# Optimization experiments

Hardware: AMD Instinct MI355X
Metric: run time of the kernel (lower is better)

The kernel has to match this reference:

```python
import jax, jax.numpy as jnp
import numpy as np

VOCAB, H, E, B, S = 50257, 1024, 1024, 64, 2048


def setup_inputs() -> dict:
    key = jax.random.key(0)
    ks = jax.random.split(key, 12)
    s = 0.02
    return {
        "input_seq": jax.random.randint(ks[0], (B,), 0, VOCAB),
        "last_hidden": jax.random.normal(ks[1], (1, B, H), jnp.float32),
        "last_cell": jax.random.normal(ks[2], (1, B, H), jnp.float32),
        "encoder_outputs": jax.random.normal(ks[3], (S, B, H), jnp.float32),
        "emb_W": jax.random.normal(ks[4], (VOCAB, E), jnp.float32) * s,
        "W_ih": jax.random.normal(ks[5], (4 * H, E), jnp.float32) * s,
        "W_hh": jax.random.normal(ks[6], (4 * H, H), jnp.float32) * s,
        "b_ih": jnp.zeros((4 * H,), jnp.float32),
        "b_hh": jnp.zeros((4 * H,), jnp.float32),
        "concat_W": jax.random.normal(ks[7], (H, 2 * H), jnp.float32) * s,
        "concat_b": jnp.zeros((H,), jnp.float32),
        "out_W": jax.random.normal(ks[8], (VOCAB, H), jnp.float32) * s,
        "out_b": jnp.zeros((VOCAB,), jnp.float32),
    }


def reference(input_seq, last_hidden, last_cell, encoder_outputs,
              emb_W, W_ih, W_hh, b_ih, b_hh,
              concat_W, concat_b, out_W, out_b):
    # Embedding lookup (dropout is identity in eval mode)
    x = emb_W[input_seq]                      # [B, E]
    h0 = last_hidden[0]                       # [B, H]
    c0 = last_cell[0]                         # [B, H]
    # Single LSTM step (PyTorch gate order: i, f, g, o)
    gates = x @ W_ih.T + b_ih + h0 @ W_hh.T + b_hh   # [B, 4H]
    i, f, g, o = jnp.split(gates, 4, axis=-1)
    c = jax.nn.sigmoid(f) * c0 + jax.nn.sigmoid(i) * jnp.tanh(g)
    h = jax.nn.sigmoid(o) * jnp.tanh(c)       # [B, H] == rnn_output
    # 'dot' attention: energies[b, s] = h[b] . enc[s, b]  (vectorized)
    energies = jnp.einsum('bh,sbh->bs', h, encoder_outputs)   # [B, S]
    attn = jax.nn.softmax(energies, axis=1)                   # [B, S]
    context = jnp.einsum('bs,sbh->bh', attn, encoder_outputs) # [B, H]
    concat_out = jnp.tanh(jnp.concatenate([h, context], axis=1) @ concat_W.T + concat_b)
    output = concat_out @ out_W.T + out_b                     # [B, VOCAB]
    return output, h[None], c[None], attn[:, None, :]
```

## Files before the change

### kernel.cpp

```cpp
#include <hip/hip_runtime.h>
#include <hip/hip_bf16.h>
#include <math.h>

#define BB 64
#define HH 1024
#define SS 2048
#define VV 50257

typedef float f32x4 __attribute__((ext_vector_type(4)));
typedef short bf16x8 __attribute__((ext_vector_type(8)));

__device__ __forceinline__ float sigf(float x){ return 1.0f/(1.0f+__expf(-x)); }
__device__ __forceinline__ short f2bf(float f){
  __hip_bfloat16 h = __float2bfloat16(f);
  return __builtin_bit_cast(short, h);
}
__device__ __forceinline__ float bf2f(short s){
  __hip_bfloat16 h = __builtin_bit_cast(__hip_bfloat16, s);
  return __bfloat162float(h);
}

__global__ void k_prep(const int* __restrict__ seq, const float* __restrict__ embW,
                       const float* __restrict__ h0,
                       short* __restrict__ Ahi, short* __restrict__ Alo){
  const int b = blockIdx.x;
  const int k = threadIdx.x * 8;
  const float* src = (k < 1024) ? (embW + (size_t)seq[b]*1024 + k)
                                : (h0 + (size_t)b*1024 + (k - 1024));
  float4 v0 = *(const float4*)src;
  float4 v1 = *(const float4*)(src + 4);
  float v[8] = {v0.x,v0.y,v0.z,v0.w,v1.x,v1.y,v1.z,v1.w};
  bf16x8 hi, lo;
  #pragma unroll
  for (int j = 0; j < 8; ++j) {
    short h = f2bf(v[j]);
    hi[j] = h;
    lo[j] = f2bf(v[j] - bf2f(h));
  }
  *(bf16x8*)(Ahi + (size_t)b*2048 + k) = hi;
  *(bf16x8*)(Alo + (size_t)b*2048 + k) = lo;
}

__global__ __launch_bounds__(256, 3)
void k_gates(const short* __restrict__ Ahi, const short* __restrict__ Alo,
             const float* __restrict__ W_ih, const float* __restrict__ W_hh,
             float* __restrict__ dst)
{
  const int tid = threadIdx.x;
  const int wave = tid >> 6, lane = tid & 63;
  const int r = lane & 15, g = lane >> 4;
  const int nb = blockIdx.x, sk = blockIdx.y;
  const int n0 = nb*128 + wave*32;
  const int kbase = sk*128;
  const float* Wm = (kbase < 1024) ? W_ih : W_hh;
  const int kw = (kbase < 1024) ? kbase : (kbase - 1024);

  f32x4 acc[4][2] = {};

  #pragma unroll
  for (int ks = 0; ks < 4; ++ks) {
    const int kk = kbase + ks*32 + g*8;
    const int ko = kw   + ks*32 + g*8;
    bf16x8 ahi[4], alo[4];
    #pragma unroll
    for (int mf = 0; mf < 4; ++mf) {
      ahi[mf] = *(const bf16x8*)(Ahi + (size_t)(mf*16 + r)*2048 + kk);
      alo[mf] = *(const bf16x8*)(Alo + (size_t)(mf*16 + r)*2048 + kk);
    }
    #pragma unroll
    for (int nf = 0; nf < 2; ++nf) {
      const int n = n0 + nf*16 + r;
      const float* wp = Wm + (size_t)n*1024 + ko;
      float4 w0 = *(const float4*)wp;
      float4 w1 = *(const float4*)(wp + 4);
      float wv[8] = {w0.x,w0.y,w0.z,w0.w,w1.x,w1.y,w1.z,w1.w};
      bf16x8 whi, wlo;
      #pragma unroll
      for (int j = 0; j < 8; ++j) {
        short h = f2bf(wv[j]);
        whi[j] = h;
        wlo[j] = f2bf(wv[j] - bf2f(h));
      }
      #pragma unroll
      for (int mf = 0; mf < 4; ++mf) {
        acc[mf][nf] = __builtin_amdgcn_mfma_f32_16x16x32_bf16(ahi[mf], whi, acc[mf][nf], 0,0,0);
        acc[mf][nf] = __builtin_amdgcn_mfma_f32_16x16x32_bf16(alo[mf], whi, acc[mf][nf], 0,0,0);
        acc[mf][nf] = __builtin_amdgcn_mfma_f32_16x16x32_bf16(ahi[mf], wlo, acc[mf][nf], 0,0,0);
      }
    }
  }

  #pragma unroll
  for (int nf = 0; nf < 2; ++nf) {
    const int n = n0 + nf*16 + r;
    #pragma unroll
    for (int mf = 0; mf < 4; ++mf)
      #pragma unroll
      for (int j = 0; j < 4; ++j)
        dst[((size_t)sk*64 + (mf*16 + g*4 + j))*4096 + n] = acc[mf][nf][j];
  }
}

__global__ void k_rlstm(const float* __restrict__ part, const float* __restrict__ b_ih,
                        const float* __restrict__ b_hh, const float* __restrict__ c0,
                        float* __restrict__ h_out, float* __restrict__ c_out,
                        short* __restrict__ concA, int SK){
  int idx = blockIdx.x*256 + threadIdx.x;
  int b = idx >> 10, k = idx & 1023;
  float gi = b_ih[k]      + b_hh[k];
  float gf = b_ih[1024+k] + b_hh[1024+k];
  float gg = b_ih[2048+k] + b_hh[2048+k];
  float go = b_ih[3072+k] + b_hh[3072+k];
  const float* p = part + (size_t)b*4096 + k;
  for (int s = 0; s < SK; ++s) {
    const float* ps = p + (size_t)s*64*4096;
    gi += ps[0]; gf += ps[1024]; gg += ps[2048]; go += ps[3072];
  }
  float c = sigf(gf)*c0[idx] + sigf(gi)*tanhf(gg);
  float h = sigf(go)*tanhf(c);
  c_out[idx] = c;
  h_out[idx] = h;
  concA[(size_t)b*2048 + k] = f2bf(h);
}

__global__ __launch_bounds__(256)
void k_mfma(const short* __restrict__ A, int lda,
            const float* __restrict__ W1, int ldw,
            float* __restrict__ dst, int N, int Ktot)
{
  const int tid  = threadIdx.x;
  const int wave = tid >> 6, lane = tid & 63;
  const int nb = blockIdx.x, sk = blockIdx.y, SK = gridDim.y;
  const int ksteps = Ktot >> 5;
  const int kps = ksteps / SK;
  const int k0 = sk * kps;
  const int n0 = nb*128 + wave*32;
  const int r = lane & 15, g = lane >> 4;

  f32x4 acc[4][2] = {};

  for (int ks = k0; ks < k0 + kps; ++ks) {
    const int kk = (ks << 5) + g*8;
    bf16x8 af[4];
    #pragma unroll
    for (int mf = 0; mf < 4; ++mf)
      af[mf] = *(const bf16x8*)(A + (size_t)(mf*16 + r)*lda + kk);
    #pragma unroll
    for (int nf = 0; nf < 2; ++nf) {
      const int n = n0 + nf*16 + r;
      const float* wp = W1 + (size_t)n*ldw + kk;
      float4 w0 = *(const float4*)wp;
      float4 w1 = *(const float4*)(wp + 4);
      bf16x8 bfr;
      bfr[0]=f2bf(w0.x); bfr[1]=f2bf(w0.y); bfr[2]=f2bf(w0.z); bfr[3]=f2bf(w0.w);
      bfr[4]=f2bf(w1.x); bfr[5]=f2bf(w1.y); bfr[6]=f2bf(w1.z); bfr[7]=f2bf(w1.w);
      #pragma unroll
      for (int mf = 0; mf < 4; ++mf)
        acc[mf][nf] = __builtin_amdgcn_mfma_f32_16x16x32_bf16(af[mf], bfr, acc[mf][nf], 0, 0, 0);
    }
  }

  #pragma unroll
  for (int nf = 0; nf < 2; ++nf) {
    const int n = n0 + nf*16 + r;
    #pragma unroll
    for (int mf = 0; mf < 4; ++mf)
      #pragma unroll
      for (int j = 0; j < 4; ++j)
        dst[((size_t)sk*64 + (mf*16 + g*4 + j))*N + n] = acc[mf][nf][j];
  }
}

__global__ void k_reduce(const float* __restrict__ part, const float* __restrict__ bias,
                         short* __restrict__ dstb, int N, int SK){
  size_t idx = (size_t)blockIdx.x*256 + threadIdx.x;
  if (idx >= (size_t)64*N) return;
  int b = (int)(idx / N), n = (int)(idx % N);
  float v = bias[n];
  for (int s = 0; s < SK; ++s) v += part[((size_t)s*64 + b)*N + n];
  dstb[(size_t)b*N + n] = f2bf(tanhf(v));
}

__global__ __launch_bounds__(256, 3)
void k_logits(const short* __restrict__ A, const float* __restrict__ W,
              const float* __restrict__ bias, float* __restrict__ out)
{
  const int tid = threadIdx.x;
  const int wave = tid >> 6, lane = tid & 63;
  const int r = lane & 15, g = lane >> 4;
  const int cg = wave & 1, kh = wave >> 1;
  const int n0 = blockIdx.x*64 + cg*32;
  const int nA = n0 + r, nB = n0 + 16 + r;
  const int nAc = (nA < VV) ? nA : 0;
  const int nBc = (nB < VV) ? nB : 0;
  const int kb = kh * 512;

  const short* A0 = A + (size_t)r*1024       + kb + g*8;
  const short* A1 = A + (size_t)(16+r)*1024  + kb + g*8;
  const short* A2 = A + (size_t)(32+r)*1024  + kb + g*8;
  const short* A3 = A + (size_t)(48+r)*1024  + kb + g*8;
  const float* wA = W + (size_t)nAc*1024 + kb + g*8;
  const float* wB = W + (size_t)nBc*1024 + kb + g*8;

  f32x4 acc[4][2] = {};

  bf16x8 aE0,aE1,aE2,aE3, aO0,aO1,aO2,aO3;
  float4 wEA0,wEA1,wEB0,wEB1, wOA0,wOA1,wOB0,wOB1;

#define LOAD_E(KS) { const int o=(KS)*32; \
    aE0=*(const bf16x8*)(A0+o); aE1=*(const bf16x8*)(A1+o); \
    aE2=*(const bf16x8*)(A2+o); aE3=*(const bf16x8*)(A3+o); \
    wEA0=*(const float4*)(wA+o); wEA1=*(const float4*)(wA+o+4); \
    wEB0=*(const float4*)(wB+o); wEB1=*(const float4*)(wB+o+4); }
#define LOAD_O(KS) { const int o=(KS)*32; \
    aO0=*(const bf16x8*)(A0+o); aO1=*(const bf16x8*)(A1+o); \
    aO2=*(const bf16x8*)(A2+o); aO3=*(const bf16x8*)(A3+o); \
    wOA0=*(const float4*)(wA+o); wOA1=*(const float4*)(wA+o+4); \
    wOB0=*(const float4*)(wB+o); wOB1=*(const float4*)(wB+o+4); }
#define CVT(bdst, w0, w1) { \
    bdst[0]=f2bf(w0.x); bdst[1]=f2bf(w0.y); bdst[2]=f2bf(w0.z); bdst[3]=f2bf(w0.w); \
    bdst[4]=f2bf(w1.x); bdst[5]=f2bf(w1.y); bdst[6]=f2bf(w1.z); bdst[7]=f2bf(w1.w); }
#define MM(a0_,a1_,a2_,a3_,bA_,bB_) { \
    acc[0][0]=__builtin_amdgcn_mfma_f32_16x16x32_bf16(a0_,bA_,acc[0][0],0,0,0); \
    acc[1][0]=__builtin_amdgcn_mfma_f32_16x16x32_bf16(a1_,bA_,acc[1][0],0,0,0); \
    acc[2][0]=__builtin_amdgcn_mfma_f32_16x16x32_bf16(a2_,bA_,acc[2][0],0,0,0); \
    acc[3][0]=__builtin_amdgcn_mfma_f32_16x16x32_bf16(a3_,bA_,acc[3][0],0,0,0); \
    acc[0][1]=__builtin_amdgcn_mfma_f32_16x16x32_bf16(a0_,bB_,acc[0][1],0,0,0); \
    acc[1][1]=__builtin_amdgcn_mfma_f32_16x16x32_bf16(a1_,bB_,acc[1][1],0,0,0); \
    acc[2][1]=__builtin_amdgcn_mfma_f32_16x16x32_bf16(a2_,bB_,acc[2][1],0,0,0); \
    acc[3][1]=__builtin_amdgcn_mfma_f32_16x16x32_bf16(a3_,bB_,acc[3][1],0,0,0); }

  LOAD_E(0);
  LOAD_O(1);
  #pragma unroll
  for (int it = 0; it < 8; ++it) {
    const int ks = it*2;
    {
      bf16x8 bA, bB;
      CVT(bA, wEA0, wEA1); CVT(bB, wEB0, wEB1);
      bf16x8 ca0=aE0, ca1=aE1, ca2=aE2, ca3=aE3;
      if (it < 7) LOAD_E(ks+2);
      MM(ca0,ca1,ca2,ca3,bA,bB);
    }
    {
      bf16x8 bA, bB;
      CVT(bA, wOA0, wOA1); CVT(bB, wOB0, wOB1);
      bf16x8 ca0=aO0, ca1=aO1, ca2=aO2, ca3=aO3;
      if (it < 7) LOAD_O(ks+3);
      MM(ca0,ca1,ca2,ca3,bA,bB);
    }
  }
#undef LOAD_E
#undef LOAD_O
#undef CVT
#undef MM

  __shared__ float red[2][32][64];
  if (kh) {
    #pragma unroll
    for (int nf = 0; nf < 2; ++nf)
      #pragma unroll
      for (int mf = 0; mf < 4; ++mf)
        #pragma unroll
        for (int j = 0; j < 4; ++j)
          red[cg][nf*16 + mf*4 + j][lane] = acc[mf][nf][j];
  }
  __syncthreads();
  if (!kh) {
    #pragma unroll
    for (int nf = 0; nf < 2; ++nf) {
      const int n = n0 + nf*16 + r;
      if (n < VV) {
        const float bv = bias[n];
        #pragma unroll
        for (int mf = 0; mf < 4; ++mf)
          #pragma unroll
          for (int j = 0; j < 4; ++j)
            out[(size_t)(mf*16 + g*4 + j)*VV + n] =
                acc[mf][nf][j] + red[cg][nf*16 + mf*4 + j][lane] + bv;
      }
    }
  }
}

__global__ __launch_bounds__(256)
void k_attn_part(const float* __restrict__ h, const float* __restrict__ enc,
                 float* __restrict__ energ, float* __restrict__ mpart,
                 float* __restrict__ lpart, float* __restrict__ ctxpart, int C){
  const int b  = blockIdx.x & 63;
  const int ch = blockIdx.x >> 6;
  const int wave = threadIdx.x >> 6;
  const int lane = threadIdx.x & 63;
  const int rows = SS / C;
  const int rpw  = rows >> 2;
  const int sw = ch*rows + wave*rpw;

  float4 hv0, hv1, hv2, hv3;
  {
    const float* hb = h + (size_t)b*HH + lane*16;
    hv0 = *(const float4*)(hb);   hv1 = *(const float4*)(hb+4);
    hv2 = *(const float4*)(hb+8); hv3 = *(const float4*)(hb+12);
  }
  float m = -INFINITY, l = 0.f;
  float cacc[16];
  #pragma unroll
  for (int j = 0; j < 16; ++j) cacc[j] = 0.f;

  for (int i = 0; i < rpw; i += 2) {
    const float* ep = enc + ((size_t)(sw+i)*BB + b)*HH + lane*16;
    const float* fp = ep + (size_t)BB*HH;
    const float4 e0 = *(const float4*)(ep);
    const float4 e1 = *(const float4*)(ep+4);
    const float4 e2 = *(const float4*)(ep+8);
    const float4 e3 = *(const float4*)(ep+12);
    const float4 f0 = *(const float4*)(fp);
    const float4 f1 = *(const float4*)(fp+4);
    const float4 f2 = *(const float4*)(fp+8);
    const float4 f3 = *(const float4*)(fp+12);
    float p = hv0.x*e0.x + hv0.y*e0.y + hv0.z*e0.z + hv0.w*e0.w
            + hv1.x*e1.x + hv1.y*e1.y + hv1.z*e1.z + hv1.w*e1.w
            + hv2.x*e2.x + hv2.y*e2.y + hv2.z*e2.z + hv2.w*e2.w
            + hv3.x*e3.x + hv3.y*e3.y + hv3.z*e3.z + hv3.w*e3.w;
    float q = hv0.x*f0.x + hv0.y*f0.y + hv0.z*f0.z + hv0.w*f0.w
            + hv1.x*f1.x + hv1.y*f1.y + hv1.z*f1.z + hv1.w*f1.w
            + hv2.x*f2.x + hv2.y*f2.y + hv2.z*f2.z + hv2.w*f2.w
            + hv3.x*f3.x + hv3.y*f3.y + hv3.z*f3.z + hv3.w*f3.w;
    p += __shfl_xor(p, 1);  q += __shfl_xor(q, 1);
    p += __shfl_xor(p, 2);  q += __shfl_xor(q, 2);
    p += __shfl_xor(p, 4);  q += __shfl_xor(q, 4);
    p += __shfl_xor(p, 8);  q += __shfl_xor(q, 8);
    p += __shfl_xor(p, 16); q += __shfl_xor(q, 16);
    p += __shfl_xor(p, 32); q += __shfl_xor(q, 32);
    if (lane == 0) {
      float2 pq; pq.x = p; pq.y = q;
      *(float2*)(energ + (size_t)b*SS + sw + i) = pq;
    }
    const float mn = fmaxf(fmaxf(m, p), q);
    const float sc = __expf(m - mn);
    const float pe = __expf(p - mn);
    const float qe = __expf(q - mn);
    l = l*sc + pe + qe;
    cacc[0] = cacc[0]*sc + pe*e0.x + qe*f0.x;
    cacc[1] = cacc[1]*sc + pe*e0.y + qe*f0.y;
    cacc[2] = cacc[2]*sc + pe*e0.z + qe*f0.z;
    cacc[3] = cacc[3]*sc + pe*e0.w + qe*f0.w;
    cacc[4] = cacc[4]*sc + pe*e1.x + qe*f1.x;
    cacc[5] = cacc[5]*sc + pe*e1.y + qe*f1.y;
    cacc[6] = cacc[6]*sc + pe*e1.z + qe*f1.z;
    cacc[7] = cacc[7]*sc + pe*e1.w + qe*f1.w;
    cacc[8] = cacc[8]*sc + pe*e2.x + qe*f2.x;
    cacc[9] = cacc[9]*sc + pe*e2.y + qe*f2.y;
    cacc[10] = cacc[10]*sc + pe*e2.z + qe*f2.z;
    cacc[11] = cacc[11]*sc + pe*e2.w + qe*f2.w;
    cacc[12] = cacc[12]*sc + pe*e3.x + qe*f3.x;
    cacc[13] = cacc[13]*sc + pe*e3.y + qe*f3.y;
    cacc[14] = cacc[14]*sc + pe*e3.z + qe*f3.z;
    cacc[15] = cacc[15]*sc + pe*e3.w + qe*f3.w;
    m = mn;
  }

  __shared__ float sm[4], sl[4];
  __shared__ float sctx[4][1024];
  if (lane == 0) { sm[wave] = m; sl[wave] = l; }
  __syncthreads();
  const float mg = fmaxf(fmaxf(sm[0], sm[1]), fmaxf(sm[2], sm[3]));
  const float lg = sl[0]*__expf(sm[0]-mg) + sl[1]*__expf(sm[1]-mg)
                 + sl[2]*__expf(sm[2]-mg) + sl[3]*__expf(sm[3]-mg);
  const float scw = __expf(m - mg);
  #pragma unroll
  for (int j = 0; j < 16; ++j) sctx[wave][lane*16 + j] = cacc[j]*scw;
  __syncthreads();
  const int d = threadIdx.x * 4;
  const float4 a0 = *(const float4*)&sctx[0][d];
  const float4 a1 = *(const float4*)&sctx[1][d];
  const float4 a2 = *(const float4*)&sctx[2][d];
  const float4 a3 = *(const float4*)&sctx[3][d];
  float4 rr;
  rr.x = a0.x+a1.x+a2.x+a3.x; rr.y = a0.y+a1.y+a2.y+a3.y;
  rr.z = a0.z+a1.z+a2.z+a3.z; rr.w = a0.w+a1.w+a2.w+a3.w;
  *(float4*)(ctxpart + ((size_t)(b*C + ch))*HH + d) = rr;
  if (threadIdx.x == 0) { mpart[b*C+ch] = mg; lpart[b*C+ch] = lg; }
}

__global__ void k_attn_fin(const float* __restrict__ mpart, const float* __restrict__ lpart,
                           const float* __restrict__ ctxpart, const float* __restrict__ energ,
                           float* __restrict__ attn, short* __restrict__ concA, int C){
  const int b = blockIdx.x, tid = threadIdx.x;
  float m = -INFINITY;
  for (int c = 0; c < C; ++c) m = fmaxf(m, mpart[b*C+c]);
  float l = 0.f;
  for (int c = 0; c < C; ++c) l += lpart[b*C+c] * __expf(mpart[b*C+c] - m);
  const float inv = 1.0f / l;
  float ax = 0.f, ay = 0.f, az = 0.f, aw = 0.f;
  for (int c = 0; c < C; ++c) {
    const float w = __expf(mpart[b*C+c] - m);
    const float* cp = ctxpart + ((size_t)(b*C+c))*HH + tid*4;
    ax += w*cp[0]; ay += w*cp[1]; az += w*cp[2]; aw += w*cp[3];
  }
  ax *= inv; ay *= inv; az *= inv; aw *= inv;
  short* ca = concA + (size_t)b*2048 + 1024 + tid*4;
  ca[0] = f2bf(ax); ca[1] = f2bf(ay); ca[2] = f2bf(az); ca[3] = f2bf(aw);
  for (int j = 0; j < 8; ++j) {
    const int s = j*256 + tid;
    attn[(size_t)b*SS + s] = __expf(energ[(size_t)b*SS + s] - m) * inv;
  }
}

extern "C" void kernel_launch(void* const* d_in, const int* in_sizes, int n_in,
                              void* d_out, int out_size, void* d_ws, size_t ws_size,
                              hipStream_t stream){
  const int*   seq  = (const int*)  d_in[0];
  const float* h0   = (const float*)d_in[1];
  const float* c0   = (const float*)d_in[2];
  const float* enc  = (const float*)d_in[3];
  const float* embW = (const float*)d_in[4];
  const float* W_ih = (const float*)d_in[5];
  const float* W_hh = (const float*)d_in[6];
  const float* b_ih = (const float*)d_in[7];
  const float* b_hh = (const float*)d_in[8];
  const float* cW   = (const float*)d_in[9];
  const float* cb   = (const float*)d_in[10];
  const float* oW   = (const float*)d_in[11];
  const float* ob   = (const float*)d_in[12];
  float* out = (float*)d_out;

  float* ws = (float*)d_ws;
  const size_t o_energ = 0;
  const size_t o_concA = 131072;
  const size_t o_concB = 196608;
  const size_t o_Ahi   = 229376;
  const size_t o_Alo   = 294912;
  const size_t o_mp    = 360448;
  const size_t SKPART  = 4194304;
  int C = 32;
  for (;;) {
    size_t need = (o_mp + (size_t)64*C*2 + (size_t)64*C*1024 + SKPART) * sizeof(float);
    if (need <= ws_size || C == 1) break;
    C >>= 1;
  }
  float* energ   = ws + o_energ;
  short* concA   = (short*)(ws + o_concA);
  short* concB   = (short*)(ws + o_concB);
  short* Ahi     = (short*)(ws + o_Ahi);
  short* Alo     = (short*)(ws + o_Alo);
  float* mpart   = ws + o_mp;
  float* lpart   = mpart + (size_t)64*C;
  float* ctxpart = lpart + (size_t)64*C;
  float* skpart  = ctxpart + (size_t)64*C*1024;

  const size_t o_h = 3216448, o_c = 3281984, o_attn = 3347520;

  k_prep<<<64, 256, 0, stream>>>(seq, embW, h0, Ahi, Alo);
  k_gates<<<dim3(32,16), 256, 0, stream>>>(Ahi, Alo, W_ih, W_hh, skpart);
  k_rlstm<<<256, 256, 0, stream>>>(skpart, b_ih, b_hh, c0, out + o_h, out + o_c,
                                   concA, 16);
  k_attn_part<<<64*C, 256, 0, stream>>>(out + o_h, enc, energ, mpart, lpart, ctxpart, C);
  k_attn_fin<<<64, 256, 0, stream>>>(mpart, lpart, ctxpart, energ, out + o_attn, concA, C);
  k_mfma<<<dim3(8,16), 256, 0, stream>>>(concA, 2048, cW, 2048, skpart, 1024, 2048);
  k_reduce<<<256, 256, 0, stream>>>(skpart, cb, concB, 1024, 16);
  k_logits<<<786, 256, 0, stream>>>(concB, oW, ob, out);
}
```

Measured before the change: 258.8 us.

## Stage logits weight tiles through double-buffered LDS with coalesced row loads

The vocab-projection kernel now has all four threads per row cooperatively load each W row in contiguous 64-element chunks, with four threads covering one row's 64-float chunk. The chunks are written into a double-buffered shared-memory tile, and each wave reads its MFMA B fragments from that tile. The previous split-K across waves, with its shared-memory reduction, is replaced by each wave owning 16 columns over the full K range. The goal is better-coalesced global reads of the large fp32 out_W stream. The cost is two barriers per K tile, no explicit A prefetch, and a dropped occupancy hint, which could hurt latency hiding.

```diff
diff --git a/kernel.cpp b/kernel.cpp
--- a/kernel.cpp
+++ b/kernel.cpp
@@ -181,105 +181,84 @@
   dstb[(size_t)b*N + n] = f2bf(tanhf(v));
 }
 
-__global__ __launch_bounds__(256, 3)
+__global__ __launch_bounds__(256)
 void k_logits(const short* __restrict__ A, const float* __restrict__ W,
               const float* __restrict__ bias, float* __restrict__ out)
 {
+  __shared__ float4 WfA[2][512];
+  __shared__ float4 WfB[2][512];
+
   const int tid = threadIdx.x;
   const int wave = tid >> 6, lane = tid & 63;
   const int r = lane & 15, g = lane >> 4;
-  const int cg = wave & 1, kh = wave >> 1;
-  const int n0 = blockIdx.x*64 + cg*32;
-  const int nA = n0 + r, nB = n0 + 16 + r;
-  const int nAc = (nA < VV) ? nA : 0;
-  const int nBc = (nB < VV) ? nB : 0;
-  const int kb = kh * 512;
-
-  const short* A0 = A + (size_t)r*1024       + kb + g*8;
-  const short* A1 = A + (size_t)(16+r)*1024  + kb + g*8;
-  const short* A2 = A + (size_t)(32+r)*1024  + kb + g*8;
-  const short* A3 = A + (size_t)(48+r)*1024  + kb + g*8;
-  const float* wA = W + (size_t)nAc*1024 + kb + g*8;
-  const float* wB = W + (size_t)nBc*1024 + kb + g*8;
-
-  f32x4 acc[4][2] = {};
-
-  bf16x8 aE0,aE1,aE2,aE3, aO0,aO1,aO2,aO3;
-  float4 wEA0,wEA1,wEB0,wEB1, wOA0,wOA1,wOB0,wOB1;
-
-#define LOAD_E(KS) { const int o=(KS)*32; \
-    aE0=*(const bf16x8*)(A0+o); aE1=*(const bf16x8*)(A1+o); \
-    aE2=*(const bf16x8*)(A2+o); aE3=*(const bf16x8*)(A3+o); \
-    wEA0=*(const float4*)(wA+o); wEA1=*(const float4*)(wA+o+4); \
-    wEB0=*(const float4*)(wB+o); wEB1=*(const float4*)(wB+o+4); }
-#define LOAD_O(KS) { const int o=(KS)*32; \
-    aO0=*(const bf16x8*)(A0+o); aO1=*(const bf16x8*)(A1+o); \
-    aO2=*(const bf16x8*)(A2+o); aO3=*(const bf16x8*)(A3+o); \
-    wOA0=*(const float4*)(wA+o); wOA1=*(const float4*)(wA+o+4); \
-    wOB0=*(const float4*)(wB+o); wOB1=*(const float4*)(wB+o+4); }
-#define CVT(bdst, w0, w1) { \
-    bdst[0]=f2bf(w0.x); bdst[1]=f2bf(w0.y); bdst[2]=f2bf(w0.z); bdst[3]=f2bf(w0.w); \
-    bdst[4]=f2bf(w1.x); bdst[5]=f2bf(w1.y); bdst[6]=f2bf(w1.z); bdst[7]=f2bf(w1.w); }
-#define MM(a0_,a1_,a2_,a3_,bA_,bB_) { \
-    acc[0][0]=__builtin_amdgcn_mfma_f32_16x16x32_bf16(a0_,bA_,acc[0][0],0,0,0); \
-    acc[1][0]=__builtin_amdgcn_mfma_f32_16x16x32_bf16(a1_,bA_,acc[1][0],0,0,0); \
-    acc[2][0]=__builtin_amdgcn_mfma_f32_16x16x32_bf16(a2_,bA_,acc[2][0],0,0,0); \
-    acc[3][0]=__builtin_amdgcn_mfma_f32_16x16x32_bf16(a3_,bA_,acc[3][0],0,0,0); \
-    acc[0][1]=__builtin_amdgcn_mfma_f32_16x16x32_bf16(a0_,bB_,acc[0][1],0,0,0); \
-    acc[1][1]=__builtin_amdgcn_mfma_f32_16x16x32_bf16(a1_,bB_,acc[1][1],0,0,0); \
-    acc[2][1]=__builtin_amdgcn_mfma_f32_16x16x32_bf16(a2_,bB_,acc[2][1],0,0,0); \
-    acc[3][1]=__builtin_amdgcn_mfma_f32_16x16x32_bf16(a3_,bB_,acc[3][1],0,0,0); }
-
-  LOAD_E(0);
-  LOAD_O(1);
-  #pragma unroll
-  for (int it = 0; it < 8; ++it) {
-    const int ks = it*2;
-    {
-      bf16x8 bA, bB;
-      CVT(bA, wEA0, wEA1); CVT(bB, wEB0, wEB1);
-      bf16x8 ca0=aE0, ca1=aE1, ca2=aE2, ca3=aE3;
-      if (it < 7) LOAD_E(ks+2);
-      MM(ca0,ca1,ca2,ca3,bA,bB);
-    }
-    {
-      bf16x8 bA, bB;
-      CVT(bA, wOA0, wOA1); CVT(bB, wOB0, wOB1);
-      bf16x8 ca0=aO0, ca1=aO1, ca2=aO2, ca3=aO3;
-      if (it < 7) LOAD_O(ks+3);
-      MM(ca0,ca1,ca2,ca3,bA,bB);
-    }
-  }
-#undef LOAD_E
-#undef LOAD_O
-#undef CVT
-#undef MM
-
-  __shared__ float red[2][32][64];
-  if (kh) {
-    #pragma unroll
-    for (int nf = 0; nf < 2; ++nf)
-      #pragma unroll
-      for (int mf = 0; mf < 4; ++mf)
-        #pragma unroll
-        for (int j = 0; j < 4; ++j)
-          red[cg][nf*16 + mf*4 + j][lane] = acc[mf][nf][j];
-  }
+  const int n0 = blockIdx.x * 64;
+  const int row64 = tid >> 2;
+  const int rowg  = (n0 + row64 < VV) ? (n0 + row64) : (VV - 1);
+  const float* wrow = W + (size_t)rowg * 1024;
+  const int wS = row64 >> 4, rS = row64 & 15;
+
+  f32x4 acc[4] = {};
+
+#define STAGE_LOAD(KT, ST) { \
+    _Pragma("unroll") \
+    for (int i = 0; i < 4; ++i) { \
+      const int kl = ((tid & 3) * 4) + i * 16; \
+      ST[i] = *(const float4*)(wrow + (KT) + kl); \
+    } }
+#define STAGE_WRITE(BUF, ST) { \
+    _Pragma("unroll") \
+    for (int i = 0; i < 4; ++i) { \
+      const int kl = ((tid & 3) * 4) + i * 16; \
+      const int ks = kl >> 5; \
+      const int gg = (kl & 31) >> 3; \
+      const int idx = ks*256 + wS*64 + gg*16 + rS; \
+      if (kl & 4) WfB[BUF][idx] = ST[i]; else WfA[BUF][idx] = ST[i]; \
+    } }
+
+  float4 st[4];
+  STAGE_LOAD(0, st);
+  STAGE_WRITE(0, st);
   __syncthreads();
-  if (!kh) {
-    #pragma unroll
-    for (int nf = 0; nf < 2; ++nf) {
-      const int n = n0 + nf*16 + r;
-      if (n < VV) {
-        const float bv = bias[n];
-        #pragma unroll
-        for (int mf = 0; mf < 4; ++mf)
-          #pragma unroll
-          for (int j = 0; j < 4; ++j)
-            out[(size_t)(mf*16 + g*4 + j)*VV + n] =
-                acc[mf][nf][j] + red[cg][nf*16 + mf*4 + j][lane] + bv;
+
+  int buf = 0;
+  for (int t = 0; t < 16; ++t) {
+    float4 st2[4];
+    if (t < 15) STAGE_LOAD((t+1)*64, st2);
+
+    const int kt = t * 64;
+    #pragma unroll
+    for (int ks = 0; ks < 2; ++ks) {
+      const float4 w0 = WfA[buf][ks*256 + tid];
+      const float4 w1 = WfB[buf][ks*256 + tid];
+      bf16x8 bfr;
+      bfr[0]=f2bf(w0.x); bfr[1]=f2bf(w0.y); bfr[2]=f2bf(w0.z); bfr[3]=f2bf(w0.w);
+      bfr[4]=f2bf(w1.x); bfr[5]=f2bf(w1.y); bfr[6]=f2bf(w1.z); bfr[7]=f2bf(w1.w);
+      const int kk = kt + ks*32 + g*8;
+      #pragma unroll
+      for (int mf = 0; mf < 4; ++mf) {
+        const bf16x8 af = *(const bf16x8*)(A + (size_t)(mf*16 + r)*1024 + kk);
+        acc[mf] = __builtin_amdgcn_mfma_f32_16x16x32_bf16(af, bfr, acc[mf], 0, 0, 0);
       }
     }
+
+    if (t < 15) {
+      __syncthreads();
+      STAGE_WRITE(buf ^ 1, st2);
+      __syncthreads();
+      buf ^= 1;
+    }
+  }
+#undef STAGE_LOAD
+#undef STAGE_WRITE
+
+  const int n = n0 + wave*16 + r;
+  if (n < VV) {
+    const float bv = bias[n];
+    #pragma unroll
+    for (int mf = 0; mf < 4; ++mf)
+      #pragma unroll
+      for (int j = 0; j < 4; ++j)
+        out[(size_t)(mf*16 + g*4 + j)*VV + n] = acc[mf][j] + bv;
   }
 }
 
```

After: 322.8 us. 1.25x slower.
